# Kernel tuning notes

Measured on AMD Instinct MI355X. Metric: run time of the kernel, lower is better.

## Reference

```python
import jax, jax.numpy as jnp
import numpy as np
from jax import lax

GN_EPS = 1e-5
LRELU_SLOPE = 0.2
TOP_K = 3
COMMITMENT = 0.25
NUM_CODES = 1024

def conv(x, w, b, stride=1, pad=1):
    y = lax.conv_general_dilated(x, w, (stride, stride), ((pad, pad), (pad, pad)),
                                 dimension_numbers=('NCHW', 'OIHW', 'NCHW'))
    return y + b[None, :, None, None]

def conv_transpose(x, w, b, stride=2, pad=1, out_pad=1):
    # torch ConvTranspose2d: w is (Cin, Cout, kH, kW); equivalent to lhs-dilated conv
    # with flipped, io-swapped kernel and padding k-1-p (plus out_pad on high side).
    k = w.shape[2]
    p = k - 1 - pad
    w_f = jnp.transpose(jnp.flip(w, (2, 3)), (1, 0, 2, 3))  # -> OIHW
    y = lax.conv_general_dilated(x, w_f, (1, 1), ((p, p + out_pad), (p, p + out_pad)),
                                 lhs_dilation=(stride, stride),
                                 dimension_numbers=('NCHW', 'OIHW', 'NCHW'))
    return y + b[None, :, None, None]

def group_norm(x, g, beta, groups=2):
    N, C, H, W = x.shape
    xg = x.reshape(N, groups, C // groups, H, W)
    mu = xg.mean((2, 3, 4), keepdims=True)
    var = xg.var((2, 3, 4), keepdims=True)
    xn = ((xg - mu) * lax.rsqrt(var + GN_EPS)).reshape(N, C, H, W)
    return xn * g[None, :, None, None] + beta[None, :, None, None]

def lrelu(x):
    return jnp.where(x >= 0, x, LRELU_SLOPE * x)

def vq_ema_eval(z, emb):
    # z: [B, D, H, W] -> tokens [N, D]; eval path (no EMA buffer updates)
    inputs = jnp.transpose(z, (0, 2, 3, 1))  # [B,H,W,D]
    flat = inputs.reshape(-1, emb.shape[1])
    d = (jnp.sum(flat ** 2, 1, keepdims=True) + jnp.sum(emb ** 2, 1)
         - 2.0 * flat @ emb.T)  # [N, K]
    _, idx = lax.top_k(-d, TOP_K)  # top_k smallest distances
    q0 = emb[idx[:, 0]].reshape(inputs.shape)
    e_latent_loss = jnp.mean((lax.stop_gradient(q0) - inputs) ** 2)
    loss = COMMITMENT * e_latent_loss
    quantized = inputs + lax.stop_gradient(q0 - inputs)  # straight-through
    # perplexity uses the LAST (k-th nearest) encodings, matching the torch loop
    last = idx[:, TOP_K - 1]
    counts = jnp.zeros((emb.shape[0],), flat.dtype).at[last].add(1.0)
    avg_probs = counts / flat.shape[0]
    perplexity = jnp.exp(-jnp.sum(avg_probs * jnp.log(avg_probs + 1e-10)))
    return loss, jnp.transpose(quantized, (0, 3, 1, 2)), perplexity

def setup_inputs() -> dict:
    key = jax.random.key(0)
    ks = jax.random.split(key, 16)
    s = 0.05
    d = {
        'x': jax.random.normal(ks[0], (4, 4, 96, 96), jnp.float32),
        'e0_w': jax.random.normal(ks[1], (128, 4, 3, 3), jnp.float32) * s,
        'e0_b': jnp.zeros((128,), jnp.float32),
        'e0_g': jnp.ones((128,), jnp.float32),
        'e0_beta': jnp.zeros((128,), jnp.float32),
        'e1_w': jax.random.normal(ks[2], (128, 128, 3, 3), jnp.float32) * s,
        'e1_b': jnp.zeros((128,), jnp.float32),
        'e1_g': jnp.ones((128,), jnp.float32),
        'e1_beta': jnp.zeros((128,), jnp.float32),
        'pv_w': jax.random.normal(ks[3], (128, 128, 1, 1), jnp.float32) * s,
        'pv_b': jnp.zeros((128,), jnp.float32),
        'emb': jax.random.normal(ks[4], (NUM_CODES, 128), jnp.float32),
        'd0_w': jax.random.normal(ks[5], (128, 128, 3, 3), jnp.float32) * s,  # ConvT: (Cin,Cout,k,k)
        'd0_b': jnp.zeros((128,), jnp.float32),
        'd0_g': jnp.ones((128,), jnp.float32),
        'd0_beta': jnp.zeros((128,), jnp.float32),
        'd1_w': jax.random.normal(ks[6], (128, 256, 3, 3), jnp.float32) * s,
        'd1_b': jnp.zeros((128,), jnp.float32),
        'd1_g': jnp.ones((128,), jnp.float32),
        'd1_beta': jnp.zeros((128,), jnp.float32),
        'proj_w': jax.random.normal(ks[7], (128, 128, 1, 1), jnp.float32) * s,
        'proj_b': jnp.zeros((128,), jnp.float32),
        'ro_w': jax.random.normal(ks[8], (4, 128, 1, 1), jnp.float32) * s,
        'ro_b': jnp.zeros((4,), jnp.float32),
    }
    return d

def reference(x, e0_w, e0_b, e0_g, e0_beta, e1_w, e1_b, e1_g, e1_beta,
              pv_w, pv_b, emb,
              d0_w, d0_b, d0_g, d0_beta, d1_w, d1_b, d1_g, d1_beta,
              proj_w, proj_b, ro_w, ro_b):
    # Encoder: strides [1, 2]
    enc1 = lrelu(group_norm(conv(x, e0_w, e0_b, stride=1, pad=1), e0_g, e0_beta))
    latent = lrelu(group_norm(conv(enc1, e1_w, e1_b, stride=2, pad=1), e1_g, e1_beta))
    z = conv(latent, pv_w, pv_b, stride=1, pad=0)
    loss, quantized, perplexity = vq_ema_eval(z, emb)
    # Decoder: strides [2, 1]; skip projected (embedding_dim != C_out)
    skip = conv(enc1, proj_w, proj_b, stride=1, pad=0)
    h = lrelu(group_norm(conv_transpose(quantized, d0_w, d0_b, stride=2, pad=1, out_pad=1), d0_g, d0_beta))
    y = lrelu(group_norm(conv(jnp.concatenate([h, skip], axis=1), d1_w, d1_b, stride=1, pad=1), d1_g, d1_beta))
    x_recon = conv(y, ro_w, ro_b, stride=1, pad=0)
    return (loss, x_recon, perplexity)
```

## Files before the change

kernel.cpp:

```cpp
#include <hip/hip_runtime.h>

#define DEVI __device__ __forceinline__

typedef unsigned short u16;
typedef __attribute__((ext_vector_type(8))) short bf8v;
typedef __attribute__((ext_vector_type(4))) short s4v;
typedef __attribute__((ext_vector_type(4))) float f4v;

constexpr int NB = 4, C = 128, H = 96, W = 96, HW = H * W;
constexpr int HL = 48, WL = 48, HWL = HL * WL;
constexpr int CODES = 1024, DIM = 128;
constexpr int ROWS = NB * HWL;

DEVI float lrelu_f(float v) { return v >= 0.f ? v : 0.2f * v; }

DEVI u16 f2bf(float f) {
  union { float f; unsigned u; } v; v.f = f;
  unsigned r = (v.u + 0x7FFFu + ((v.u >> 16) & 1u)) >> 16;
  return (u16)r;
}

DEVI float bf2f(u16 h) {
  union { unsigned u; float f; } v; v.u = (unsigned)h << 16;
  return v.f;
// ... 13 lines not shown
  if (threadIdx.x == 0) {
    s = ls[0] + ls[1] + ls[2] + ls[3];
    s2 = ls2[0] + ls2[1] + ls2[2] + ls2[3];
    return true;
  }
  return false;
}

DEVI void ins3(float e, int j, float& d0, int& i0, float& d1, int& i1, float& d2, int& i2) {
  bool b0 = (e < d0) || (e == d0 && j < i0);
  bool b1 = (e < d1) || (e == d1 && j < i1);
  bool b2 = (e < d2) || (e == d2 && j < i2);
  float nd0 = b0 ? e : d0;             int ni0 = b0 ? j : i0;
  float nd1 = b0 ? d0 : (b1 ? e : d1); int ni1 = b0 ? i0 : (b1 ? j : i1);
  float nd2 = b1 ? d1 : (b2 ? e : d2); int ni2 = b1 ? i1 : (b2 ? j : i2);
  d0 = nd0; i0 = ni0; d1 = nd1; i1 = ni1; d2 = nd2; i2 = ni2;
}

__global__ __launch_bounds__(256) void k_red16(const float2* __restrict__ src,
                                               float* __restrict__ dst, int per) {
  int slot = blockIdx.x;
  float s = 0.f, s2 = 0.f;
  for (int i = threadIdx.x; i < per; i += 256) {
    float2 v = src[(size_t)slot * per + i];
    s += v.x; s2 += v.y;
  }
  if (block_red2(s, s2)) { dst[slot * 2] = s; dst[slot * 2 + 1] = s2; }
}

__global__ __launch_bounds__(256) void k_pack_all(
    const float* __restrict__ d1_w, const float* __restrict__ d0_w,
    const float* __restrict__ pj_w, const float* __restrict__ emb,
    const float* __restrict__ e1_w,
    u16* __restrict__ A1, u16* __restrict__ A0, u16* __restrict__ Apj,
    u16* __restrict__ ehtil, u16* __restrict__ We1,
    float* __restrict__ enorm, float* __restrict__ counts) {
  int b = blockIdx.x, t = threadIdx.x;
  if (b < 1152) {
    int i = b * 256 + t;
    int ci = i & 31, co = (i >> 5) & 127, r = i >> 12;
    int kx = r % 3; int r2 = r / 3; int ch = r2 & 7, ky = r2 >> 3;
    A1[i] = f2bf(d1_w[((size_t)(co * 256 + ch * 32 + ci) * 3 + ky) * 3 + kx]);
  } else if (b < 1728) {
    int i = (b - 1152) * 256 + t;
    int ci = i & 31, co = (i >> 5) & 127, r = i >> 12;
    int wx = r % 3; int r2 = r / 3; int ch = r2 & 3, wy = r2 >> 2;
    A0[i] = f2bf(d0_w[((size_t)((ch * 32 + ci) * 128 + co) * 3 + wy) * 3 + wx]);
  } else if (b < 1792) {
    int i = (b - 1728) * 256 + t;
    int ci = i & 31, co = (i >> 5) & 127, ch = i >> 12;
    Apj[i] = f2bf(pj_w[co * 128 + ch * 32 + ci]);
  } else if (b < 1920) {
    int g = (b - 1792) * 256 + t;
    int ct = g >> 9; int rem = g & 511;
    int j = rem >> 6; int l = rem & 63;
    int code = ct * 16 + (l & 15);
    int kb = j * 32 + (l >> 4) * 8;
    bool lo = kb >= 128; int k0 = lo ? kb - 128 : kb;
    const float* ep = emb + (size_t)code * DIM + k0;
    u16 o[8];
#pragma unroll
    for (int e = 0; e < 8; ++e) {
      float v = ep[e];
      u16 h = f2bf(v);
      o[e] = lo ? f2bf(v - bf2f(h)) : h;
    }
    bf8v ov = {(short)o[0], (short)o[1], (short)o[2], (short)o[3],
               (short)o[4], (short)o[5], (short)o[6], (short)o[7]};
    *(bf8v*)&ehtil[(size_t)g * 8] = ov;
  } else if (b < 1924) {
    int e = (b - 1920) * 256 + t;
    const float4* p = (const float4*)(emb + (size_t)e * DIM);
    float s = 0.f;
#pragma unroll 8
    for (int i = 0; i < 32; ++i) {
      float4 v = p[i];
      s = fmaf(v.x, v.x, s); s = fmaf(v.y, v.y, s); s = fmaf(v.z, v.z, s); s = fmaf(v.w, v.w, s);
    }
    enorm[e] = s;
  } else if (b == 1924) {
#pragma unroll
    for (int k = 0; k < 4; ++k) counts[t + k * 256] = 0.f;
  } else {
    int p = (b - 1925) * 256 + t;
    int s = p >> 6, l = p & 63;
    int ct = s & 7; int r = s >> 3;
    int kx = r % 3; int r2 = r / 3; int ch = r2 & 3, ky = r2 >> 2;
    int co = ct * 16 + (l & 15), ci0 = ch * 32 + (l >> 4) * 8;
    u16 hh[8], ll[8];
#pragma unroll
    for (int e = 0; e < 8; ++e) {
      float v = e1_w[((size_t)(co * 128 + ci0 + e) * 3 + ky) * 3 + kx];
      u16 h = f2bf(v); hh[e] = h; ll[e] = f2bf(v - bf2f(h));
    }
    bf8v hv = {(short)hh[0], (short)hh[1], (short)hh[2], (short)hh[3],
               (short)hh[4], (short)hh[5], (short)hh[6], (short)hh[7]};
    bf8v lv = {(short)ll[0], (short)ll[1], (short)ll[2], (short)ll[3],
               (short)ll[4], (short)ll[5], (short)ll[6], (short)ll[7]};
    *(bf8v*)&We1[(size_t)s * 1024 + l * 8] = hv;
    *(bf8v*)&We1[(size_t)s * 1024 + 512 + l * 8] = lv;
  }
}

__global__ __launch_bounds__(256) void k_conv_e0t(
    const float* __restrict__ x, const float* __restrict__ wg,
    const float* __restrict__ bias, float* __restrict__ out, float2* __restrict__ ps) {
  __shared__ float xs[4][18][104];
  int b = blockIdx.x;
  int rq = b % 6; int co = (b / 6) & 127; int n = b / 768;
  int t = threadIdx.x;
  int tx = t & 15, r = t >> 4;
  int y0 = rq * 16;
  for (int e = t; e < 4 * 18 * 104; e += 256) {
    int ci = e / 1872; int rem = e - ci * 1872;
    int row = rem / 104; int off = rem - row * 104;
    int iy = y0 - 1 + row; int ix = off - 1;
    float v = 0.f;
    if ((unsigned)iy < 96u && (unsigned)ix < 96u)
      v = x[((size_t)(n * 4 + ci)) * HW + iy * 96 + ix];
    xs[ci][row][off] = v;
  }
  float wr[4][9];
  const float* wp = wg + co * 36;
#pragma unroll
  for (int ci = 0; ci < 4; ++ci)
#pragma unroll
    for (int k = 0; k < 9; ++k) wr[ci][k] = wp[ci * 9 + k];
  float bv = bias[co];
  __syncthreads();
  float acc[6];
#pragma unroll
  for (int p = 0; p < 6; ++p) acc[p] = bv;
#pragma unroll
// ... 107 lines not shown
        acc[nt] = __builtin_amdgcn_mfma_f32_16x16x32_bf16(ah[0], bho0, acc[nt], 0, 0, 0);
        acc[nt] = __builtin_amdgcn_mfma_f32_16x16x32_bf16(al[0], bho0, acc[nt], 0, 0, 0);
        acc[nt] = __builtin_amdgcn_mfma_f32_16x16x32_bf16(ah[0], blo0, acc[nt], 0, 0, 0);
        acc[nt] = __builtin_amdgcn_mfma_f32_16x16x32_bf16(ah[2], bho1, acc[nt], 0, 0, 0);
        acc[nt] = __builtin_amdgcn_mfma_f32_16x16x32_bf16(al[2], bho1, acc[nt], 0, 0, 0);
        acc[nt] = __builtin_amdgcn_mfma_f32_16x16x32_bf16(ah[2], blo1, acc[nt], 0, 0, 0);
      }
    }
  }
  int co0 = cb * 64 + w * 16 + quad * 4;
  float4 bv = *(const float4*)&bias[co0];
  float s = 0.f, s2 = 0.f;
#pragma unroll
  for (int nt = 0; nt < 3; ++nt) {
    int px = nt * 16 + ln16;
#pragma unroll
    for (int g = 0; g < 4; ++g) {
      float bvg = (g == 0) ? bv.x : (g == 1) ? bv.y : (g == 2) ? bv.z : bv.w;
      float v = acc[nt][g] + bvg;
      latent[((size_t)(n * 128 + co0 + g)) * 2304 + oy * 48 + px] = v;
      s += v; s2 += v * v;
    }
  }
  wave_red2(s, s2);
  if (lane == 0) { ls[w] = s; ls2[w] = s2; }
  __syncthreads();
  if (t == 0) {
    int slot = n * 2 + cb;
    ps[(size_t)slot * 48 + oy] =
        make_float2(ls[0] + ls[1] + ls[2] + ls[3], ls2[0] + ls2[1] + ls2[2] + ls2[3]);
  }
}

__global__ __launch_bounds__(256) void k_gn_nhwc_bf(
    const float* __restrict__ in, u16* __restrict__ outb, const float* __restrict__ stats,
    const float* __restrict__ gam, const float* __restrict__ bet) {
  int idx = blockIdx.x * 256 + threadIdx.x;
  int c = idx & 127;
  int n = idx / (9216 * 128);
  const float* st = stats + (n * 2 + (c >> 6)) * 2;
  const float invcnt = 1.f / (64.f * 9216.f);
  float mu = st[0] * invcnt;
  float var = fmaf(-mu, mu, st[1] * invcnt);
  float rs = rsqrtf(var + 1e-5f);
  float v = in[idx];
  outb[idx] = f2bf(lrelu_f(fmaf((v - mu) * rs, gam[c], bet[c])));
}

__global__ __launch_bounds__(256, 2) void k_pv(
    const float* __restrict__ in, const float* __restrict__ w,
    const float* __restrict__ bias, const float* __restrict__ stats1,
    const float* __restrict__ gam, const float* __restrict__ bet,
    u16* __restrict__ zp) {
  int b = blockIdx.x;
  int pxb = b % 36; int cb = (b / 36) & 1; int n = b / 72;
  int t = threadIdx.x;
  int pxg = t & 7, cg = t >> 3;
  int px0 = pxb * 64 + pxg * 8;
  int cobase = cb * 64 + cg * 2;
  const float invc = 1.f / (64.f * 2304.f);
  float acc[2][8];
#pragma unroll
  for (int c = 0; c < 2; ++c) {
    float bv = bias[cobase + c];
#pragma unroll
    for (int p = 0; p < 8; ++p) acc[c][p] = bv;
  }
  const float* ipb = in + (size_t)n * 128 * HWL + px0;
  for (int ci0 = 0; ci0 < 128; ci0 += 4) {
    float inr[4][8];
#pragma unroll
    for (int i = 0; i < 4; ++i) {
      int c = ci0 + i;
      const float* st = stats1 + (n * 2 + (c >> 6)) * 2;
      float mu = st[0] * invc;
      float var = fmaf(-mu, mu, st[1] * invc);
      float rsv = rsqrtf(var + 1e-5f);
      float ga = gam[c], be = bet[c];
      const float* ip = ipb + (size_t)c * HWL;
// ... 5 lines not shown
      inr[i][4] = lrelu_f(fmaf((bq.x - mu) * rsv, ga, be));
      inr[i][5] = lrelu_f(fmaf((bq.y - mu) * rsv, ga, be));
      inr[i][6] = lrelu_f(fmaf((bq.z - mu) * rsv, ga, be));
      inr[i][7] = lrelu_f(fmaf((bq.w - mu) * rsv, ga, be));
    }
    float wr[2][4];
#pragma unroll
    for (int c = 0; c < 2; ++c) {
      float4 wv = *(const float4*)&w[(size_t)(cobase + c) * 128 + ci0];
      wr[c][0] = wv.x; wr[c][1] = wv.y; wr[c][2] = wv.z; wr[c][3] = wv.w;
    }
#pragma unroll
    for (int i = 0; i < 4; ++i)
#pragma unroll
      for (int c = 0; c < 2; ++c)
#pragma unroll
        for (int p = 0; p < 8; ++p) acc[c][p] = fmaf(wr[c][i], inr[i][p], acc[c][p]);
  }
#pragma unroll
  for (int p = 0; p < 8; ++p) {
    size_t r = (size_t)n * HWL + px0 + p;
    u16 h0 = f2bf(acc[0][p]); u16 l0 = f2bf(acc[0][p] - bf2f(h0));
    u16 h1 = f2bf(acc[1][p]); u16 l1 = f2bf(acc[1][p] - bf2f(h1));
    unsigned hp = (unsigned)h0 | ((unsigned)h1 << 16);
    unsigned lp = (unsigned)l0 | ((unsigned)l1 << 16);
    *(unsigned*)&zp[r * 256 + cobase] = hp;
    *(unsigned*)&zp[r * 256 + 128 + cobase] = lp;
  }
}

__global__ __launch_bounds__(512, 4) void k_vq(
    const u16* __restrict__ zp, const u16* __restrict__ ehtil,
    const float* __restrict__ emb, const float* __restrict__ enorm,
    u16* __restrict__ qb, float* __restrict__ counts, float* __restrict__ pvq) {
  __shared__ float wd[8][16][3];
  __shared__ int   wi[8][16][3];
  __shared__ float lred[8];
  __shared__ int hist[CODES];
  int r0 = blockIdx.x * 16;
  int t = threadIdx.x, w = t >> 6, lane = t & 63;
  int ln16 = lane & 15, quad = lane >> 4;
  hist[t] = 0; hist[t + 512] = 0;
  const u16* zrow = zp + (size_t)(r0 + ln16) * 256 + quad * 8;
  bf8v bh[4], bl[4];
#pragma unroll
  for (int kk = 0; kk < 4; ++kk) {
    bh[kk] = *(const bf8v*)(zrow + kk * 32);
    bl[kk] = *(const bf8v*)(zrow + 128 + kk * 32);
  }
  float d0 = 3.4e38f, d1 = 3.4e38f, d2 = 3.4e38f;
  int i0 = -1, i1 = -1, i2 = -1;
  const u16* abase = ehtil + (size_t)(w * 8) * 4096 + lane * 8;
#pragma unroll
  for (int tt = 0; tt < 8; ++tt) {
    const u16* ap = abase + tt * 4096;
    bf8v af[8];
#pragma unroll
    for (int j = 0; j < 8; ++j) af[j] = *(const bf8v*)(ap + j * 512);
    f4v accA = (f4v){0.f, 0.f, 0.f, 0.f};
    f4v accB = (f4v){0.f, 0.f, 0.f, 0.f};
    f4v accC = (f4v){0.f, 0.f, 0.f, 0.f};
#pragma unroll
    for (int kk = 0; kk < 4; ++kk) {
      accA = __builtin_amdgcn_mfma_f32_16x16x32_bf16(af[kk], bh[kk], accA, 0, 0, 0);
      accB = __builtin_amdgcn_mfma_f32_16x16x32_bf16(af[4 + kk], bh[kk], accB, 0, 0, 0);
      accC = __builtin_amdgcn_mfma_f32_16x16x32_bf16(af[kk], bl[kk], accC, 0, 0, 0);
    }
// ... 12 lines not shown
  }
#pragma unroll
  for (int off = 16; off <= 32; off <<= 1) {
    float e0 = __shfl_xor(d0, off), e1 = __shfl_xor(d1, off), e2 = __shfl_xor(d2, off);
    int j0 = __shfl_xor(i0, off), j1 = __shfl_xor(i1, off), j2 = __shfl_xor(i2, off);
    ins3(e0, j0, d0, i0, d1, i1, d2, i2);
    ins3(e1, j1, d0, i0, d1, i1, d2, i2);
    ins3(e2, j2, d0, i0, d1, i1, d2, i2);
  }
  if (quad == 0) {
    wd[w][ln16][0] = d0; wd[w][ln16][1] = d1; wd[w][ln16][2] = d2;
    wi[w][ln16][0] = i0; wi[w][ln16][1] = i1; wi[w][ln16][2] = i2;
  }
  __syncthreads();
  float lsum = 0.f;
  for (int ii = 0; ii < 2; ++ii) {
    int i = w * 2 + ii;
    float bd; int bi;
    if (lane < 24) { bd = wd[lane / 3][i][lane % 3]; bi = wi[lane / 3][i][lane % 3]; }
    else { bd = 3.4e38f; bi = 0x7fffffff; }
    int a[3];
#pragma unroll
    for (int p = 0; p < 3; ++p) {
      float d = bd; int idx = bi;
#pragma unroll
      for (int o = 1; o <= 32; o <<= 1) {
        float od = __shfl_xor(d, o); int oi = __shfl_xor(idx, o);
        if (od < d || (od == d && oi < idx)) { d = od; idx = oi; }
      }
      a[p] = idx;
      if (bi == idx) { bd = 3.4e38f; bi = 0x7fffffff; }
    }
    int r = r0 + i;
    const float* q0p = emb + (size_t)a[0] * DIM;
    const u16* zr = zp + (size_t)r * 256;
    float lp = 0.f;
#pragma unroll
    for (int cc = 0; cc < 2; ++cc) {
      int c = lane + cc * 64;
      float qv = q0p[c];
      qb[(size_t)r * 128 + c] = f2bf(qv);
      float zv = bf2f(zr[c]) + bf2f(zr[128 + c]);
      float dd = zv - qv;
      lp = fmaf(dd, dd, lp);
    }
#pragma unroll
    for (int o = 32; o > 0; o >>= 1) lp += __shfl_down(lp, o);
    if (lane == 0) { lsum += lp; atomicAdd(&hist[a[2]], 1); }
  }
  if (lane == 0) lred[w] = lsum;
  __syncthreads();
  if (t == 0) {
    float s = 0.f;
#pragma unroll
    for (int q = 0; q < 8; ++q) s += lred[q];
    pvq[blockIdx.x] = s;
  }
#pragma unroll
  for (int k = 0; k < 2; ++k) {
    int e = t + k * 512;
    int cnt = hist[e];
    if (cnt) atomicAdd(&counts[e], (float)cnt);
  }
}

__global__ __launch_bounds__(256) void k_finalize(
    const float* __restrict__ counts, const float* __restrict__ pvq, float* __restrict__ out) {
  float local = 0.f;
#pragma unroll
  for (int k = 0; k < 4; ++k) {
    float cnt = counts[threadIdx.x + k * 256];
    float pr = cnt * (1.f / (float)ROWS);
    local = fmaf(pr, logf(pr + 1e-10f), local);
  }
  float lsum = 0.f;
  for (int i = threadIdx.x; i < ROWS / 16; i += 256) lsum += pvq[i];
  if (block_red2(local, lsum)) {
    out[1 + NB * 4 * HW] = expf(-local);
    out[0] = 0.25f * lsum * (1.f / (9216.f * 128.f));
  }
}

__global__ __launch_bounds__(256) void k_proj_m(
    const float* __restrict__ enc1, const u16* __restrict__ Apj,
    const float* __restrict__ bias, const float* __restrict__ stats0,
    const float* __restrict__ gam, const float* __restrict__ bet,
    u16* __restrict__ skipb) {
  __shared__ u16 Ash[128 * 32];
  __shared__ u16 Bsh[96 * 32];
  int b = blockIdx.x; int rowi = b % 96; int n = b / 96; int px0 = rowi * 96;
  int t = threadIdx.x; int w = t >> 6; int lane = t & 63;
  int ln16 = lane & 15, quad = lane >> 4;
  int co0w = (w & 1) * 64; int pxh = (w >> 1) * 48;
  int c_l = t & 31, xg = t >> 5;
  const float invc = 1.f / (64.f * 9216.f);
  f4v acc[4][3];
#pragma unroll
  for (int mt = 0; mt < 4; ++mt)
#pragma unroll
    for (int nt = 0; nt < 3; ++nt) acc[mt][nt] = (f4v){0.f, 0.f, 0.f, 0.f};
  for (int ch = 0; ch < 4; ++ch) {
    __syncthreads();
#pragma unroll
    for (int e = 0; e < 2; ++e) {
      int i = t + e * 256;
      *(bf8v*)&Ash[i * 8] = *(const bf8v*)&Apj[ch * 4096 + i * 8];
    }
    int c = ch * 32 + c_l;
    const float* st = stats0 + (n * 2 + (ch >> 1)) * 2;
    float mu = st[0] * invc;
    float var = fmaf(-mu, mu, st[1] * invc);
    float rsv = rsqrtf(var + 1e-5f);
    float ga = gam[c], be = bet[c];
    const float* ip = enc1 + (size_t)(n * 128 + c) * 9216 + px0 + xg * 12;
#pragma unroll
    for (int j4 = 0; j4 < 3; ++j4) {
      float4 v = *(const float4*)(ip + j4 * 4);
      int pxb = xg * 12 + j4 * 4;
      Bsh[(pxb + 0) * 32 + c_l] = f2bf(lrelu_f(fmaf((v.x - mu) * rsv, ga, be)));
      Bsh[(pxb + 1) * 32 + c_l] = f2bf(lrelu_f(fmaf((v.y - mu) * rsv, ga, be)));
      Bsh[(pxb + 2) * 32 + c_l] = f2bf(lrelu_f(fmaf((v.z - mu) * rsv, ga, be)));
      Bsh[(pxb + 3) * 32 + c_l] = f2bf(lrelu_f(fmaf((v.w - mu) * rsv, ga, be)));
    }
    __syncthreads();
    bf8v af[4];
#pragma unroll
    for (int mt = 0; mt < 4; ++mt)
      af[mt] = *(const bf8v*)&Ash[(co0w + mt * 16 + ln16) * 32 + quad * 8];
#pragma unroll
    for (int nt = 0; nt < 3; ++nt) {
      bf8v bfv = *(const bf8v*)&Bsh[(pxh + nt * 16 + ln16) * 32 + quad * 8];
#pragma unroll
      for (int mt = 0; mt < 4; ++mt)
        acc[mt][nt] = __builtin_amdgcn_mfma_f32_16x16x32_bf16(af[mt], bfv, acc[mt][nt], 0, 0, 0);
    }
  }
#pragma unroll
  for (int mt = 0; mt < 4; ++mt) {
    int co = co0w + mt * 16 + quad * 4;
    float4 bv = *(const float4*)&bias[co];
#pragma unroll
    for (int nt = 0; nt < 3; ++nt) {
      int px = px0 + pxh + nt * 16 + ln16;
      u16* dp = skipb + (size_t)(n * 9216 + px) * 128 + co;
      s4v sv;
      sv.x = (short)f2bf(acc[mt][nt].x + bv.x);
      sv.y = (short)f2bf(acc[mt][nt].y + bv.y);
      sv.z = (short)f2bf(acc[mt][nt].z + bv.z);
      sv.w = (short)f2bf(acc[mt][nt].w + bv.w);
      *(s4v*)dp = sv;
    }
  }
}

__global__ __launch_bounds__(256) void k_convt_d0m(
    const u16* __restrict__ qb, const u16* __restrict__ A0,
    const float* __restrict__ bias, float* __restrict__ h, float2* __restrict__ ps) {
  __shared__ u16 Ash[2 * 128 * 32];
  __shared__ u16 Bsh[49 * 32];
  int b = blockIdx.x; int rx = b & 1; int oy = (b >> 1) % 96; int n = b / 192;
  int t = threadIdx.x; int w = t >> 6; int lane = t & 63;
  int ln16 = lane & 15, quad = lane >> 4;
  int co0w = w * 32;
  f4v acc[2][3];
#pragma unroll
  for (int mt = 0; mt < 2; ++mt)
#pragma unroll
    for (int nt = 0; nt < 3; ++nt) acc[mt][nt] = (f4v){0.f, 0.f, 0.f, 0.f};
  int nyt, wys[2], iys[2];
  if (oy & 1) {
    wys[0] = 2; iys[0] = (oy - 1) >> 1;
    wys[1] = 0; iys[1] = (oy + 1) >> 1;
    nyt = (iys[1] < 48) ? 2 : 1;
  } else { wys[0] = 1; iys[0] = oy >> 1; wys[1] = 0; iys[1] = 0; nyt = 1; }
  int nxt = rx ? 2 : 1;
  int wxs[2], xof[2];
  if (rx) { wxs[0] = 2; xof[0] = 0; wxs[1] = 0; xof[1] = 1; }
  else { wxs[0] = 1; xof[0] = 0; wxs[1] = 0; xof[1] = 0; }
  for (int yt = 0; yt < nyt; ++yt) {
    for (int ch = 0; ch < 4; ++ch) {
      __syncthreads();
      for (int e = t; e < nxt * 512; e += 256) {
        int xt = e >> 9, e2 = e & 511;
        const u16* Asrc = A0 + (size_t)(((wys[yt] * 4 + ch) * 3 + wxs[xt]) * 4096);
        *(bf8v*)&Ash[xt * 4096 + e2 * 8] = *(const bf8v*)&Asrc[e2 * 8];
      }
      const u16* bbase = qb + (size_t)(n * 2304 + iys[yt] * 48) * 128 + ch * 32;
      for (int e = t; e < 196; e += 256) {
        int row = e >> 2, seg = e & 3;
        bf8v v = {0, 0, 0, 0, 0, 0, 0, 0};
        if (row < 48) v = *(const bf8v*)&bbase[row * 128 + seg * 8];
        *(bf8v*)&Bsh[row * 32 + seg * 8] = v;
      }
      __syncthreads();
      for (int xt = 0; xt < nxt; ++xt) {
        bf8v af[2];
#pragma unroll
        for (int mt = 0; mt < 2; ++mt)
          af[mt] = *(const bf8v*)&Ash[xt * 4096 + (co0w + mt * 16 + ln16) * 32 + quad * 8];
#pragma unroll
        for (int nt = 0; nt < 3; ++nt) {
          bf8v bfv = *(const bf8v*)&Bsh[(nt * 16 + ln16 + xof[xt]) * 32 + quad * 8];
#pragma unroll
          for (int mt = 0; mt < 2; ++mt)
            acc[mt][nt] = __builtin_amdgcn_mfma_f32_16x16x32_bf16(af[mt], bfv, acc[mt][nt], 0, 0, 0);
        }
      }
    }
  }
  float s = 0.f, s2 = 0.f;
#pragma unroll
  for (int mt = 0; mt < 2; ++mt) {
    int co = co0w + mt * 16 + quad * 4;
    float4 bv = *(const float4*)&bias[co];
#pragma unroll
    for (int nt = 0; nt < 3; ++nt) {
      int px = nt * 16 + ln16;
      int ox = 2 * px + rx;
      float4 v;
      v.x = acc[mt][nt].x + bv.x; v.y = acc[mt][nt].y + bv.y;
      v.z = acc[mt][nt].z + bv.z; v.w = acc[mt][nt].w + bv.w;
      *(float4*)(h + (size_t)(n * 9216 + oy * 96 + ox) * 128 + co) = v;
      s += v.x + v.y + v.z + v.w;
      s2 += v.x * v.x + v.y * v.y + v.z * v.z + v.w * v.w;
    }
  }
  wave_red2(s, s2);
  if (lane == 0) {
    int slot = n * 2 + (w >> 1);
    ps[(size_t)slot * 384 + (oy * 2 + rx) * 2 + (w & 1)] = make_float2(s, s2);
  }
}

__global__ __launch_bounds__(256) void k_conv_d1m(
    const u16* __restrict__ hb, const u16* __restrict__ sb,
    const u16* __restrict__ A1, const float* __restrict__ bias,
    float* __restrict__ y, float2* __restrict__ ps) {
  __shared__ u16 Ash[3 * 64 * 32];
  __shared__ u16 Bsh[98 * 32];
  int b = blockIdx.x; int cb = b & 1; int oy = (b >> 1) % 96; int n = b / 192;
  int t = threadIdx.x; int w = t >> 6; int lane = t & 63;
  int ln16 = lane & 15, quad = lane >> 4;
  int co0w = (w & 1) * 32; int pxh = (w >> 1) * 48;
  f4v acc[2][3];
#pragma unroll
  for (int mt = 0; mt < 2; ++mt)
#pragma unroll
    for (int nt = 0; nt < 3; ++nt) acc[mt][nt] = (f4v){0.f, 0.f, 0.f, 0.f};
  int ky0 = (oy == 0) ? 1 : 0, ky1 = (oy == 95) ? 1 : 2;
  for (int ky = ky0; ky <= ky1; ++ky) {
    int iy = oy + ky - 1;
    for (int ch = 0; ch < 8; ++ch) {
      const u16* src = (ch < 4) ? hb : sb;
      int c0 = (ch & 3) * 32;
      const u16* Asrc = A1 + (size_t)(ky * 8 + ch) * 12288;
      const u16* bbase = src + (size_t)(n * 9216 + iy * 96) * 128 + c0;
      __syncthreads();
#pragma unroll
      for (int j = 0; j < 3; ++j) {
        int e = t + j * 256;
        int kx = e >> 8; int e2 = e & 255; int co_l = e2 >> 2; int seg = e2 & 3;
        *(bf8v*)&Ash[(kx * 64 + co_l) * 32 + seg * 8] =
            *(const bf8v*)&Asrc[(size_t)kx * 4096 + (cb * 64 + co_l) * 32 + seg * 8];
      }
      for (int e = t; e < 392; e += 256) {
        int row = e >> 2, seg = e & 3;
        int ix = row - 1;
        bf8v v = {0, 0, 0, 0, 0, 0, 0, 0};
        if ((unsigned)ix < 96u) v = *(const bf8v*)&bbase[ix * 128 + seg * 8];
        *(bf8v*)&Bsh[row * 32 + seg * 8] = v;
      }
      __syncthreads();
#pragma unroll
      for (int kx = 0; kx < 3; ++kx) {
        bf8v af[2];
#pragma unroll
        for (int mt = 0; mt < 2; ++mt)
          af[mt] = *(const bf8v*)&Ash[(kx * 64 + co0w + mt * 16 + ln16) * 32 + quad * 8];
#pragma unroll
        for (int nt = 0; nt < 3; ++nt) {
          bf8v bfv = *(const bf8v*)&Bsh[(pxh + nt * 16 + ln16 + kx) * 32 + quad * 8];
#pragma unroll
          for (int mt = 0; mt < 2; ++mt)
            acc[mt][nt] = __builtin_amdgcn_mfma_f32_16x16x32_bf16(af[mt], bfv, acc[mt][nt], 0, 0, 0);
        }
      }
    }
  }
  float s = 0.f, s2 = 0.f;
#pragma unroll
  for (int mt = 0; mt < 2; ++mt) {
    int co = cb * 64 + co0w + mt * 16 + quad * 4;
    float4 bv = *(const float4*)&bias[co];
#pragma unroll
    for (int nt = 0; nt < 3; ++nt) {
      int px = pxh + nt * 16 + ln16;
      float4 v;
      v.x = acc[mt][nt].x + bv.x; v.y = acc[mt][nt].y + bv.y;
      v.z = acc[mt][nt].z + bv.z; v.w = acc[mt][nt].w + bv.w;
      *(float4*)(y + (size_t)(n * 9216 + oy * 96 + px) * 128 + co) = v;
      s += v.x + v.y + v.z + v.w;
      s2 += v.x * v.x + v.y * v.y + v.z * v.z + v.w * v.w;
    }
  }
  wave_red2(s, s2);
  if (lane == 0) {
    int slot = n * 2 + cb;
    ps[(size_t)slot * 384 + oy * 4 + w] = make_float2(s, s2);
  }
}

__global__ __launch_bounds__(256) void k_ro(
    const float* __restrict__ y, const float* __restrict__ w,
    const float* __restrict__ bias, const float* __restrict__ stats3,
    const float* __restrict__ gam, const float* __restrict__ bet,
    float* __restrict__ out) {
  __shared__ float wsh[512];
  __shared__ float gsh[128], bsh[128];
  __shared__ float red[64][16];
  int b = blockIdx.x; int n = b / 144; int px0 = (b % 144) * 64;
  int t = threadIdx.x; int q = t & 3, pxl = t >> 2;
  for (int e = t; e < 512; e += 256) wsh[e] = w[e];
  if (t < 128) { gsh[t] = gam[t]; bsh[t] = bet[t]; }
  __syncthreads();
  const float invc = 1.f / (64.f * 9216.f);
  int g = q >> 1;
  const float* st = stats3 + (n * 2 + g) * 2;
  float mu = st[0] * invc;
  float var = fmaf(-mu, mu, st[1] * invc);
  float rsv = rsqrtf(var + 1e-5f);
  const float* yb = y + (size_t)(n * 9216 + px0 + pxl) * 128 + q * 32;
  float s0 = 0.f, s1 = 0.f, s2 = 0.f, s3 = 0.f;
#pragma unroll
  for (int j = 0; j < 8; ++j) {
    float4 v = *(const float4*)(yb + j * 4);
    int c0 = q * 32 + j * 4;
// ... 27 lines not shown
  const float* e0_g  = (const float*)d_in[3];
  const float* e0_bt = (const float*)d_in[4];
  const float* e1_w  = (const float*)d_in[5];
  const float* e1_b  = (const float*)d_in[6];
  const float* e1_g  = (const float*)d_in[7];
  const float* e1_bt = (const float*)d_in[8];
  const float* pv_w  = (const float*)d_in[9];
  const float* pv_b  = (const float*)d_in[10];
  const float* emb   = (const float*)d_in[11];
  const float* d0_w  = (const float*)d_in[12];
  const float* d0_b  = (const float*)d_in[13];
  const float* d0_g  = (const float*)d_in[14];
  const float* d0_bt = (const float*)d_in[15];
  const float* d1_w  = (const float*)d_in[16];
  const float* d1_b  = (const float*)d_in[17];
  const float* d1_g  = (const float*)d_in[18];
  const float* d1_bt = (const float*)d_in[19];
  const float* pj_w  = (const float*)d_in[20];
  const float* pj_b  = (const float*)d_in[21];
  const float* ro_w  = (const float*)d_in[22];
  const float* ro_b  = (const float*)d_in[23];
  float* out = (float*)d_out;
  float* ws = (float*)d_ws;

  float* stats  = ws;
  float* counts = ws + 64;
  float* enorm  = ws + 1088;
  float* pvq    = ws + 2112;
  float2* ps_e0 = (float2*)(ws + 3264);
  float2* ps_e1 = (float2*)(ws + 76992);
  float2* ps_d0 = (float2*)(ws + 95424);
  float2* ps_d1 = (float2*)(ws + 107712);
  float* enc1   = ws + 114688;
  float* latent = enc1 + (size_t)NB * C * HW;
  float* zbuf   = latent + (size_t)NB * C * HWL;
  float* hy     = zbuf + (size_t)NB * C * HWL;
  u16* qb    = (u16*)(hy + (size_t)NB * C * HW);
  u16* hb    = qb + (size_t)NB * C * HWL;
  u16* skipb = hb + (size_t)NB * C * HW;
  u16* A1    = skipb + (size_t)NB * C * HW;
  u16* A0    = A1 + 294912;
  u16* Apj   = A0 + 147456;
  u16* ehtil = Apj + 16384 + 64;
  u16* zp    = (u16*)zbuf;
  u16* xp  = qb;
  u16* We1 = qb + 9535488;

  k_pack_all<<<2069, 256, 0, stream>>>(d1_w, d0_w, pj_w, emb, e1_w,
                                       A1, A0, Apj, ehtil, We1, enorm, counts);

  k_conv_e0t<<<3072, 256, 0, stream>>>(x, e0_w, e0_b, enc1, ps_e0);
  k_red16<<<8, 256, 0, stream>>>(ps_e0, stats + 0, 384);
  k_gn_px<<<NB * 96 * 4, 256, 0, stream>>>(enc1, stats + 0, e0_g, e0_bt, xp);
  k_conv_e1m<<<NB * 48 * 2, 256, 0, stream>>>(xp, We1, e1_b, latent, ps_e1);
  k_red16<<<8, 256, 0, stream>>>(ps_e1, stats + 16, 48);
  k_pv<<<288, 256, 0, stream>>>(latent, pv_w, pv_b, stats + 16, e1_g, e1_bt, zp);
  k_vq<<<ROWS / 16, 512, 0, stream>>>(zp, ehtil, emb, enorm, qb, counts, pvq);
  k_finalize<<<1, 256, 0, stream>>>(counts, pvq, out);

  k_proj_m<<<NB * 96, 256, 0, stream>>>(enc1, Apj, pj_b, stats + 0, e0_g, e0_bt, skipb);
  k_convt_d0m<<<NB * 96 * 2, 256, 0, stream>>>(qb, A0, d0_b, hy, ps_d0);
  k_red16<<<8, 256, 0, stream>>>(ps_d0, stats + 32, 384);
  k_gn_nhwc_bf<<<NB * C * HW / 256, 256, 0, stream>>>(hy, hb, stats + 32, d0_g, d0_bt);
  k_conv_d1m<<<NB * 96 * 2, 256, 0, stream>>>(hb, skipb, A1, d1_b, hy, ps_d1);
  k_red16<<<8, 256, 0, stream>>>(ps_d1, stats + 48, 384);
  k_ro<<<NB * 144, 256, 0, stream>>>(hy, ro_w, ro_b, stats + 48, d1_g, d1_bt, out);
}
```

Measured before the change: 354.8 us.

## Use padded channel-chunked layouts so decoder convs read MFMA fragments from global memory

The decoder activations (quantized codes, GN'd d0 output, skip projection) are now written into padded per-row, per-32-channel chunk layouts, and the d0/d1 weights are pre-packed in MFMA fragment order. The transposed conv and the d1 conv drop their shared-memory staging and __syncthreads, loading A and B fragments directly from global/L2 with halo padding baked into the layout. The d1 conv also reassigns work so each wave covers 16 output channels across all 96 pixels. This removes LDS copies and barriers, at the cost of more uncoalesced global/L2 loads and repeated reads of the same data across waves.

```diff
diff --git a/kernel.cpp b/kernel.cpp
--- a/kernel.cpp
+++ b/kernel.cpp
@@ -69,26 +69,42 @@
     const float* __restrict__ d1_w, const float* __restrict__ d0_w,
     const float* __restrict__ pj_w, const float* __restrict__ emb,
     const float* __restrict__ e1_w,
-    u16* __restrict__ A1, u16* __restrict__ A0, u16* __restrict__ Apj,
+    u16* __restrict__ A1t, u16* __restrict__ A0t, u16* __restrict__ Apj,
     u16* __restrict__ ehtil, u16* __restrict__ We1,
-    float* __restrict__ enorm, float* __restrict__ counts) {
+    float* __restrict__ enorm, float* __restrict__ counts, u16* __restrict__ qbC) {
   int b = blockIdx.x, t = threadIdx.x;
-  if (b < 1152) {
-    int i = b * 256 + t;
-    int ci = i & 31, co = (i >> 5) & 127, r = i >> 12;
+  if (b < 144) {
+    int g = b * 256 + t;
+    int s = g >> 6, l = g & 63;
+    int ct = s & 7; int r = s >> 3;
     int kx = r % 3; int r2 = r / 3; int ch = r2 & 7, ky = r2 >> 3;
-    A1[i] = f2bf(d1_w[((size_t)(co * 256 + ch * 32 + ci) * 3 + ky) * 3 + kx]);
-  } else if (b < 1728) {
-    int i = (b - 1152) * 256 + t;
-    int ci = i & 31, co = (i >> 5) & 127, r = i >> 12;
+    int co = ct * 16 + (l & 15), ci0 = (l >> 4) * 8;
+    u16 o[8];
+#pragma unroll
+    for (int e = 0; e < 8; ++e)
+      o[e] = f2bf(d1_w[((size_t)(co * 256 + ch * 32 + ci0 + e) * 3 + ky) * 3 + kx]);
+    bf8v ov = {(short)o[0], (short)o[1], (short)o[2], (short)o[3],
+               (short)o[4], (short)o[5], (short)o[6], (short)o[7]};
+    *(bf8v*)&A1t[(size_t)g * 8] = ov;
+  } else if (b < 216) {
+    int g = (b - 144) * 256 + t;
+    int s = g >> 6, l = g & 63;
+    int ct = s & 7; int r = s >> 3;
     int wx = r % 3; int r2 = r / 3; int ch = r2 & 3, wy = r2 >> 2;
-    A0[i] = f2bf(d0_w[((size_t)((ch * 32 + ci) * 128 + co) * 3 + wy) * 3 + wx]);
-  } else if (b < 1792) {
-    int i = (b - 1728) * 256 + t;
+    int co = ct * 16 + (l & 15), ci0 = (l >> 4) * 8;
+    u16 o[8];
+#pragma unroll
+    for (int e = 0; e < 8; ++e)
+      o[e] = f2bf(d0_w[(((size_t)(ch * 32 + ci0 + e) * 128 + co) * 3 + wy) * 3 + wx]);
+    bf8v ov = {(short)o[0], (short)o[1], (short)o[2], (short)o[3],
+               (short)o[4], (short)o[5], (short)o[6], (short)o[7]};
+    *(bf8v*)&A0t[(size_t)g * 8] = ov;
+  } else if (b < 280) {
+    int i = (b - 216) * 256 + t;
     int ci = i & 31, co = (i >> 5) & 127, ch = i >> 12;
     Apj[i] = f2bf(pj_w[co * 128 + ch * 32 + ci]);
-  } else if (b < 1920) {
-    int g = (b - 1792) * 256 + t;
+  } else if (b < 408) {
+    int g = (b - 280) * 256 + t;
     int ct = g >> 9; int rem = g & 511;
     int j = rem >> 6; int l = rem & 63;
     int code = ct * 16 + (l & 15);
@@ -105,8 +121,8 @@
     bf8v ov = {(short)o[0], (short)o[1], (short)o[2], (short)o[3],
                (short)o[4], (short)o[5], (short)o[6], (short)o[7]};
     *(bf8v*)&ehtil[(size_t)g * 8] = ov;
-  } else if (b < 1924) {
-    int e = (b - 1920) * 256 + t;
+  } else if (b < 412) {
+    int e = (b - 408) * 256 + t;
     const float4* p = (const float4*)(emb + (size_t)e * DIM);
     float s = 0.f;
 #pragma unroll 8
@@ -115,11 +131,11 @@
       s = fmaf(v.x, v.x, s); s = fmaf(v.y, v.y, s); s = fmaf(v.z, v.z, s); s = fmaf(v.w, v.w, s);
     }
     enorm[e] = s;
-  } else if (b == 1924) {
+  } else if (b == 412) {
 #pragma unroll
     for (int k = 0; k < 4; ++k) counts[t + k * 256] = 0.f;
-  } else {
-    int p = (b - 1925) * 256 + t;
+  } else if (b < 557) {
+    int p = (b - 413) * 256 + t;
     int s = p >> 6, l = p & 63;
     int ct = s & 7; int r = s >> 3;
     int kx = r % 3; int r2 = r / 3; int ch = r2 & 3, ky = r2 >> 2;
@@ -136,6 +152,14 @@
                (short)ll[4], (short)ll[5], (short)ll[6], (short)ll[7]};
     *(bf8v*)&We1[(size_t)s * 1024 + l * 8] = hv;
     *(bf8v*)&We1[(size_t)s * 1024 + 512 + l * 8] = lv;
+  } else {
+    bf8v z = {0, 0, 0, 0, 0, 0, 0, 0};
+#pragma unroll
+    for (int j = 0; j < 12; ++j) {
+      int idx = t + j * 256;
+      int row = idx >> 2, q = idx & 3;
+      *(bf8v*)&qbC[(size_t)row * 1568 + 1536 + q * 8] = z;
+    }
   }
 }
 
@@ -309,19 +333,39 @@
   }
 }
 
-__global__ __launch_bounds__(256) void k_gn_nhwc_bf(
-    const float* __restrict__ in, u16* __restrict__ outb, const float* __restrict__ stats,
-    const float* __restrict__ gam, const float* __restrict__ bet) {
-  int idx = blockIdx.x * 256 + threadIdx.x;
-  int c = idx & 127;
-  int n = idx / (9216 * 128);
-  const float* st = stats + (n * 2 + (c >> 6)) * 2;
-  const float invcnt = 1.f / (64.f * 9216.f);
-  float mu = st[0] * invcnt;
-  float var = fmaf(-mu, mu, st[1] * invcnt);
+__global__ __launch_bounds__(256) void k_gn_hb(
+    const float* __restrict__ hy, const float* __restrict__ stats,
+    const float* __restrict__ gam, const float* __restrict__ bet, u16* __restrict__ hbC) {
+  int b = blockIdx.x;
+  int ch = b & 3; int iy = (b >> 2) % 96; int n = b / 384;
+  int t = threadIdx.x;
+  const float invc = 1.f / (64.f * 9216.f);
+  int g = ch >> 1;
+  const float* st = stats + (n * 2 + g) * 2;
+  float mu = st[0] * invc;
+  float var = fmaf(-mu, mu, st[1] * invc);
   float rs = rsqrtf(var + 1e-5f);
-  float v = in[idx];
-  outb[idx] = f2bf(lrelu_f(fmaf((v - mu) * rs, gam[c], bet[c])));
+  u16* chunk = hbC + ((size_t)((n * 96 + iy) * 4 + ch)) * 3136;
+  for (int e = t; e < 392; e += 256) {
+    int oct = e / 98, u = e - oct * 98;
+    int x = u - 1;
+    u16* d = chunk + u * 32 + oct * 8;
+    if ((unsigned)x >= 96u) {
+      bf8v z = {0, 0, 0, 0, 0, 0, 0, 0};
+      *(bf8v*)d = z;
+      continue;
+    }
+    const float* sp = hy + ((size_t)(n * 9216 + iy * 96 + x)) * 128 + ch * 32 + oct * 8;
+    u16 o[8];
+#pragma unroll
+    for (int e8 = 0; e8 < 8; ++e8) {
+      int c = ch * 32 + oct * 8 + e8;
+      o[e8] = f2bf(lrelu_f(fmaf((sp[e8] - mu) * rs, gam[c], bet[c])));
+    }
+    bf8v ov = {(short)o[0], (short)o[1], (short)o[2], (short)o[3],
+               (short)o[4], (short)o[5], (short)o[6], (short)o[7]};
+    *(bf8v*)d = ov;
+  }
 }
 
 __global__ __launch_bounds__(256, 2) void k_pv(
@@ -393,7 +437,7 @@
 __global__ __launch_bounds__(512, 4) void k_vq(
     const u16* __restrict__ zp, const u16* __restrict__ ehtil,
     const float* __restrict__ emb, const float* __restrict__ enorm,
-    u16* __restrict__ qb, float* __restrict__ counts, float* __restrict__ pvq) {
+    u16* __restrict__ qbC, float* __restrict__ counts, float* __restrict__ pvq) {
   __shared__ float wd[8][16][3];
   __shared__ int   wi[8][16][3];
   __shared__ float lred[8];
@@ -472,6 +516,7 @@
       if (bi == idx) { bd = 3.4e38f; bi = 0x7fffffff; }
     }
     int r = r0 + i;
+    int nn = r / 2304; int rem = r - nn * 2304; int iyL = rem / 48; int xL = rem - iyL * 48;
     const float* q0p = emb + (size_t)a[0] * DIM;
     const u16* zr = zp + (size_t)r * 256;
     float lp = 0.f;
@@ -479,7 +524,8 @@
     for (int cc = 0; cc < 2; ++cc) {
       int c = lane + cc * 64;
       float qv = q0p[c];
-      qb[(size_t)r * 128 + c] = f2bf(qv);
+      int ch = c >> 5, ci = c & 31;
+      qbC[((size_t)((nn * 48 + iyL) * 4 + ch)) * 1568 + xL * 32 + ci] = f2bf(qv);
       float zv = bf2f(zr[c]) + bf2f(zr[128 + c]);
       float dd = zv - qv;
       lp = fmaf(dd, dd, lp);
@@ -525,7 +571,7 @@
     const float* __restrict__ enc1, const u16* __restrict__ Apj,
     const float* __restrict__ bias, const float* __restrict__ stats0,
     const float* __restrict__ gam, const float* __restrict__ bet,
-    u16* __restrict__ skipb) {
+    u16* __restrict__ sbC) {
   __shared__ u16 Ash[128 * 32];
   __shared__ u16 Bsh[96 * 32];
   int b = blockIdx.x; int rowi = b % 96; int n = b / 96; int px0 = rowi * 96;
@@ -534,6 +580,12 @@
   int co0w = (w & 1) * 64; int pxh = (w >> 1) * 48;
   int c_l = t & 31, xg = t >> 5;
   const float invc = 1.f / (64.f * 9216.f);
+  if (t < 8) {
+    int chS = t >> 1, side = t & 1;
+    u16* bp = sbC + ((size_t)((n * 96 + rowi) * 4 + chS)) * 3136 + (side ? 97 : 0) * 32;
+    bf8v z = {0, 0, 0, 0, 0, 0, 0, 0};
+    *(bf8v*)bp = z; *(bf8v*)(bp + 8) = z; *(bf8v*)(bp + 16) = z; *(bf8v*)(bp + 24) = z;
+  }
   f4v acc[4][3];
 #pragma unroll
   for (int mt = 0; mt < 4; ++mt)
@@ -578,26 +630,24 @@
 #pragma unroll
   for (int mt = 0; mt < 4; ++mt) {
     int co = co0w + mt * 16 + quad * 4;
+    int chS = co >> 5, cil = co & 31;
     float4 bv = *(const float4*)&bias[co];
 #pragma unroll
     for (int nt = 0; nt < 3; ++nt) {
-      int px = px0 + pxh + nt * 16 + ln16;
-      u16* dp = skipb + (size_t)(n * 9216 + px) * 128 + co;
+      int pxl = pxh + nt * 16 + ln16;
       s4v sv;
       sv.x = (short)f2bf(acc[mt][nt].x + bv.x);
       sv.y = (short)f2bf(acc[mt][nt].y + bv.y);
       sv.z = (short)f2bf(acc[mt][nt].z + bv.z);
       sv.w = (short)f2bf(acc[mt][nt].w + bv.w);
-      *(s4v*)dp = sv;
+      *(s4v*)&sbC[((size_t)((n * 96 + rowi) * 4 + chS)) * 3136 + (pxl + 1) * 32 + cil] = sv;
     }
   }
 }
 
 __global__ __launch_bounds__(256) void k_convt_d0m(
-    const u16* __restrict__ qb, const u16* __restrict__ A0,
+    const u16* __restrict__ qbC, const u16* __restrict__ A0t,
     const float* __restrict__ bias, float* __restrict__ h, float2* __restrict__ ps) {
-  __shared__ u16 Ash[2 * 128 * 32];
-  __shared__ u16 Bsh[49 * 32];
   int b = blockIdx.x; int rx = b & 1; int oy = (b >> 1) % 96; int n = b / 192;
   int t = threadIdx.x; int w = t >> 6; int lane = t & 63;
   int ln16 = lane & 15, quad = lane >> 4;
@@ -619,31 +669,19 @@
   else { wxs[0] = 1; xof[0] = 0; wxs[1] = 0; xof[1] = 0; }
   for (int yt = 0; yt < nyt; ++yt) {
     for (int ch = 0; ch < 4; ++ch) {
-      __syncthreads();
-      for (int e = t; e < nxt * 512; e += 256) {
-        int xt = e >> 9, e2 = e & 511;
-        const u16* Asrc = A0 + (size_t)(((wys[yt] * 4 + ch) * 3 + wxs[xt]) * 4096);
-        *(bf8v*)&Ash[xt * 4096 + e2 * 8] = *(const bf8v*)&Asrc[e2 * 8];
-      }
-      const u16* bbase = qb + (size_t)(n * 2304 + iys[yt] * 48) * 128 + ch * 32;
-      for (int e = t; e < 196; e += 256) {
-        int row = e >> 2, seg = e & 3;
-        bf8v v = {0, 0, 0, 0, 0, 0, 0, 0};
-        if (row < 48) v = *(const bf8v*)&bbase[row * 128 + seg * 8];
-        *(bf8v*)&Bsh[row * 32 + seg * 8] = v;
-      }
-      __syncthreads();
+      const u16* chunk = qbC + ((size_t)((n * 48 + iys[yt]) * 4 + ch)) * 1568;
       for (int xt = 0; xt < nxt; ++xt) {
-        bf8v af[2];
+        bf8v a[2];
 #pragma unroll
         for (int mt = 0; mt < 2; ++mt)
-          af[mt] = *(const bf8v*)&Ash[xt * 4096 + (co0w + mt * 16 + ln16) * 32 + quad * 8];
+          a[mt] = *(const bf8v*)&A0t[((size_t)(((wys[yt] * 4 + ch) * 3 + wxs[xt]) * 8 + w * 2 + mt)) * 512 + lane * 8];
 #pragma unroll
         for (int nt = 0; nt < 3; ++nt) {
-          bf8v bfv = *(const bf8v*)&Bsh[(nt * 16 + ln16 + xof[xt]) * 32 + quad * 8];
+          int row = nt * 16 + ln16 + xof[xt];
+          bf8v bb = *(const bf8v*)&chunk[row * 32 + quad * 8];
 #pragma unroll
           for (int mt = 0; mt < 2; ++mt)
-            acc[mt][nt] = __builtin_amdgcn_mfma_f32_16x16x32_bf16(af[mt], bfv, acc[mt][nt], 0, 0, 0);
+            acc[mt][nt] = __builtin_amdgcn_mfma_f32_16x16x32_bf16(a[mt], bb, acc[mt][nt], 0, 0, 0);
         }
       }
     }
@@ -673,75 +711,51 @@
 }
 
 __global__ __launch_bounds__(256) void k_conv_d1m(
-    const u16* __restrict__ hb, const u16* __restrict__ sb,
-    const u16* __restrict__ A1, const float* __restrict__ bias,
+    const u16* __restrict__ hbC, const u16* __restrict__ sbC,
+    const u16* __restrict__ A1t, const float* __restrict__ bias,
     float* __restrict__ y, float2* __restrict__ ps) {
-  __shared__ u16 Ash[3 * 64 * 32];
-  __shared__ u16 Bsh[98 * 32];
   int b = blockIdx.x; int cb = b & 1; int oy = (b >> 1) % 96; int n = b / 192;
   int t = threadIdx.x; int w = t >> 6; int lane = t & 63;
   int ln16 = lane & 15, quad = lane >> 4;
-  int co0w = (w & 1) * 32; int pxh = (w >> 1) * 48;
-  f4v acc[2][3];
-#pragma unroll
-  for (int mt = 0; mt < 2; ++mt)
-#pragma unroll
-    for (int nt = 0; nt < 3; ++nt) acc[mt][nt] = (f4v){0.f, 0.f, 0.f, 0.f};
-  int ky0 = (oy == 0) ? 1 : 0, ky1 = (oy == 95) ? 1 : 2;
-  for (int ky = ky0; ky <= ky1; ++ky) {
+  f4v acc[6];
+#pragma unroll
+  for (int nt = 0; nt < 6; ++nt) acc[nt] = (f4v){0.f, 0.f, 0.f, 0.f};
+  for (int ky = 0; ky < 3; ++ky) {
     int iy = oy + ky - 1;
+    if ((unsigned)iy >= 96u) continue;
     for (int ch = 0; ch < 8; ++ch) {
-      const u16* src = (ch < 4) ? hb : sb;
-      int c0 = (ch & 3) * 32;
-      const u16* Asrc = A1 + (size_t)(ky * 8 + ch) * 12288;
-      const u16* bbase = src + (size_t)(n * 9216 + iy * 96) * 128 + c0;
-      __syncthreads();
-#pragma unroll
-      for (int j = 0; j < 3; ++j) {
-        int e = t + j * 256;
-        int kx = e >> 8; int e2 = e & 255; int co_l = e2 >> 2; int seg = e2 & 3;
-        *(bf8v*)&Ash[(kx * 64 + co_l) * 32 + seg * 8] =
-            *(const bf8v*)&Asrc[(size_t)kx * 4096 + (cb * 64 + co_l) * 32 + seg * 8];
+      const u16* chunk = (ch < 4)
+          ? hbC + ((size_t)((n * 96 + iy) * 4 + ch)) * 3136
+          : sbC + ((size_t)((n * 96 + iy) * 4 + (ch - 4))) * 3136;
+      bf8v a[3];
+#pragma unroll
+      for (int kx = 0; kx < 3; ++kx)
+        a[kx] = *(const bf8v*)&A1t[((size_t)(((ky * 8 + ch) * 3 + kx) * 8 + cb * 4 + w)) * 512 + lane * 8];
+#pragma unroll
+      for (int nt = 0; nt < 6; ++nt) {
+        int px = nt * 16 + ln16;
+        const u16* bp = chunk + px * 32 + quad * 8;
+        bf8v b0 = *(const bf8v*)bp;
+        bf8v b1 = *(const bf8v*)(bp + 32);
+        bf8v b2 = *(const bf8v*)(bp + 64);
+        acc[nt] = __builtin_amdgcn_mfma_f32_16x16x32_bf16(a[0], b0, acc[nt], 0, 0, 0);
+        acc[nt] = __builtin_amdgcn_mfma_f32_16x16x32_bf16(a[1], b1, acc[nt], 0, 0, 0);
+        acc[nt] = __builtin_amdgcn_mfma_f32_16x16x32_bf16(a[2], b2, acc[nt], 0, 0, 0);
       }
-      for (int e = t; e < 392; e += 256) {
-        int row = e >> 2, seg = e & 3;
-        int ix = row - 1;
-        bf8v v = {0, 0, 0, 0, 0, 0, 0, 0};
-        if ((unsigned)ix < 96u) v = *(const bf8v*)&bbase[ix * 128 + seg * 8];
-        *(bf8v*)&Bsh[row * 32 + seg * 8] = v;
-      }
-      __syncthreads();
-#pragma unroll
-      for (int kx = 0; kx < 3; ++kx) {
-        bf8v af[2];
-#pragma unroll
-        for (int mt = 0; mt < 2; ++mt)
-          af[mt] = *(const bf8v*)&Ash[(kx * 64 + co0w + mt * 16 + ln16) * 32 + quad * 8];
-#pragma unroll
-        for (int nt = 0; nt < 3; ++nt) {
-          bf8v bfv = *(const bf8v*)&Bsh[(pxh + nt * 16 + ln16 + kx) * 32 + quad * 8];
-#pragma unroll
-          for (int mt = 0; mt < 2; ++mt)
-            acc[mt][nt] = __builtin_amdgcn_mfma_f32_16x16x32_bf16(af[mt], bfv, acc[mt][nt], 0, 0, 0);
-        }
-      }
-    }
-  }
+    }
+  }
+  int co0 = cb * 64 + w * 16 + quad * 4;
+  float4 bv = *(const float4*)&bias[co0];
   float s = 0.f, s2 = 0.f;
 #pragma unroll
-  for (int mt = 0; mt < 2; ++mt) {
-    int co = cb * 64 + co0w + mt * 16 + quad * 4;
-    float4 bv = *(const float4*)&bias[co];
-#pragma unroll
-    for (int nt = 0; nt < 3; ++nt) {
-      int px = pxh + nt * 16 + ln16;
-      float4 v;
-      v.x = acc[mt][nt].x + bv.x; v.y = acc[mt][nt].y + bv.y;
-      v.z = acc[mt][nt].z + bv.z; v.w = acc[mt][nt].w + bv.w;
-      *(float4*)(y + (size_t)(n * 9216 + oy * 96 + px) * 128 + co) = v;
-      s += v.x + v.y + v.z + v.w;
-      s2 += v.x * v.x + v.y * v.y + v.z * v.z + v.w * v.w;
-    }
+  for (int nt = 0; nt < 6; ++nt) {
+    int px = nt * 16 + ln16;
+    float4 v;
+    v.x = acc[nt].x + bv.x; v.y = acc[nt].y + bv.y;
+    v.z = acc[nt].z + bv.z; v.w = acc[nt].w + bv.w;
+    *(float4*)(y + (size_t)(n * 9216 + oy * 96 + px) * 128 + co0) = v;
+    s += v.x + v.y + v.z + v.w;
+    s2 += v.x * v.x + v.y * v.y + v.z * v.z + v.w * v.w;
   }
   wave_red2(s, s2);
   if (lane == 0) {
@@ -835,22 +849,22 @@
   float2* ps_d0 = (float2*)(ws + 95424);
   float2* ps_d1 = (float2*)(ws + 107712);
   float* enc1   = ws + 114688;
-  float* latent = enc1 + (size_t)NB * C * HW;
-  float* zbuf   = latent + (size_t)NB * C * HWL;
-  float* hy     = zbuf + (size_t)NB * C * HWL;
-  u16* qb    = (u16*)(hy + (size_t)NB * C * HW);
-  u16* hb    = qb + (size_t)NB * C * HWL;
-  u16* skipb = hb + (size_t)NB * C * HW;
-  u16* A1    = skipb + (size_t)NB * C * HW;
-  u16* A0    = A1 + 294912;
-  u16* Apj   = A0 + 147456;
+  float* latent = enc1 + 4718592;
+  float* zbuf   = latent + 1179648;
+  float* hy     = zbuf + 1179648;
+  u16* qbC   = (u16*)(hy + 4718592);
+  u16* hbC   = qbC + 1204224;
+  u16* sbC   = hbC + 4816896;
+  u16* A1t   = sbC + 4816896;
+  u16* A0t   = A1t + 294912;
+  u16* Apj   = A0t + 147456;
   u16* ehtil = Apj + 16384 + 64;
   u16* zp    = (u16*)zbuf;
-  u16* xp  = qb;
-  u16* We1 = qb + 9535488;
-
-  k_pack_all<<<2069, 256, 0, stream>>>(d1_w, d0_w, pj_w, emb, e1_w,
-                                       A1, A0, Apj, ehtil, We1, enorm, counts);
+  u16* xp    = ehtil + 262144 + 64;
+  u16* We1   = xp + 9535488;
+
+  k_pack_all<<<558, 256, 0, stream>>>(d1_w, d0_w, pj_w, emb, e1_w,
+                                      A1t, A0t, Apj, ehtil, We1, enorm, counts, qbC);
 
   k_conv_e0t<<<3072, 256, 0, stream>>>(x, e0_w, e0_b, enc1, ps_e0);
   k_red16<<<8, 256, 0, stream>>>(ps_e0, stats + 0, 384);
@@ -858,14 +872,14 @@
   k_conv_e1m<<<NB * 48 * 2, 256, 0, stream>>>(xp, We1, e1_b, latent, ps_e1);
   k_red16<<<8, 256, 0, stream>>>(ps_e1, stats + 16, 48);
   k_pv<<<288, 256, 0, stream>>>(latent, pv_w, pv_b, stats + 16, e1_g, e1_bt, zp);
-  k_vq<<<ROWS / 16, 512, 0, stream>>>(zp, ehtil, emb, enorm, qb, counts, pvq);
+  k_vq<<<ROWS / 16, 512, 0, stream>>>(zp, ehtil, emb, enorm, qbC, counts, pvq);
   k_finalize<<<1, 256, 0, stream>>>(counts, pvq, out);
 
-  k_proj_m<<<NB * 96, 256, 0, stream>>>(enc1, Apj, pj_b, stats + 0, e0_g, e0_bt, skipb);
-  k_convt_d0m<<<NB * 96 * 2, 256, 0, stream>>>(qb, A0, d0_b, hy, ps_d0);
+  k_proj_m<<<NB * 96, 256, 0, stream>>>(enc1, Apj, pj_b, stats + 0, e0_g, e0_bt, sbC);
+  k_convt_d0m<<<NB * 96 * 2, 256, 0, stream>>>(qbC, A0t, d0_b, hy, ps_d0);
   k_red16<<<8, 256, 0, stream>>>(ps_d0, stats + 32, 384);
-  k_gn_nhwc_bf<<<NB * C * HW / 256, 256, 0, stream>>>(hy, hb, stats + 32, d0_g, d0_bt);
-  k_conv_d1m<<<NB * 96 * 2, 256, 0, stream>>>(hb, skipb, A1, d1_b, hy, ps_d1);
+  k_gn_hb<<<NB * 96 * 4, 256, 0, stream>>>(hy, stats + 32, d0_g, d0_bt, hbC);
+  k_conv_d1m<<<NB * 96 * 2, 256, 0, stream>>>(hbC, sbC, A1t, d1_b, hy, ps_d1);
   k_red16<<<8, 256, 0, stream>>>(ps_d1, stats + 48, 384);
   k_ro<<<NB * 144, 256, 0, stream>>>(hy, ro_w, ro_b, stats + 48, d1_g, d1_bt, out);
 }
```

Result: slower. 393.8 us (+11.0%).
